# Kernel optimization log

Hardware: AMD Instinct MI355X
Metric: run time of the kernel (lower is better)

Reference implementation:

```python
import jax, jax.numpy as jnp
import numpy as np

N = 100000
E = 1600000
IN_C = 128
OUT_C = 64
HID = 2 * OUT_C  # 128


def gcn_conv(x, src, dst, W, b, n):
    # PyG GCNConv with add_self_loops=True, symmetric normalization, bias.
    h = x @ W  # [n, d_out] - transform first (PyG order)
    ones = jnp.ones(src.shape[0], dtype=h.dtype)
    deg = jax.ops.segment_sum(ones, dst, num_segments=n)  # includes self-loops -> deg >= 1
    dinv = jax.lax.rsqrt(deg)
    norm = dinv[src] * dinv[dst]  # [E+n]
    msg = h[src] * norm[:, None]  # gather + scale
    return jax.ops.segment_sum(msg, dst, num_segments=n) + b


def setup_inputs() -> dict:
    key = jax.random.key(0)
    ks = jax.random.split(key, 8)
    x = jax.random.normal(ks[0], (N, IN_C), dtype=jnp.float32)
    edge_index = jax.random.randint(ks[1], (2, E), 0, N, dtype=jnp.int64)
    s1 = 1.0 / np.sqrt(IN_C)
    s2 = 1.0 / np.sqrt(HID)
    s3 = 1.0 / np.sqrt(OUT_C)
    W1 = jax.random.normal(ks[2], (IN_C, HID), dtype=jnp.float32) * s1
    b1 = jnp.zeros((HID,), dtype=jnp.float32)
    W2 = jax.random.normal(ks[3], (HID, OUT_C), dtype=jnp.float32) * s2
    b2 = jnp.zeros((OUT_C,), dtype=jnp.float32)
    Wfc = jax.random.normal(ks[4], (OUT_C, OUT_C), dtype=jnp.float32) * s3
    bfc = jax.random.uniform(ks[5], (OUT_C,), dtype=jnp.float32, minval=-s3, maxval=s3)
    return {"x": x, "edge_index": edge_index, "W1": W1, "b1": b1,
            "W2": W2, "b2": b2, "Wfc": Wfc, "bfc": bfc}


def reference(x, edge_index, W1, b1, W2, b2, Wfc, bfc):
    n = x.shape[0]
    loop = jnp.arange(n, dtype=edge_index.dtype)
    src = jnp.concatenate([edge_index[0], loop])  # add self-loops
    dst = jnp.concatenate([edge_index[1], loop])
    h = jax.nn.relu(gcn_conv(x, src, dst, W1, b1, n))
    h = gcn_conv(h, src, dst, W2, b2, n)
    return h @ Wfc + bfc
```

## Files before the change

kernel.cpp:

```cpp
#include <hip/hip_runtime.h>

#define INC  128
#define HIDC 128
#define OUTC 64

#define BSH   8
#define NBMAX 512
#define HB    128
#define TILE  4096
#define CAP   8192

typedef unsigned int  u32;
typedef unsigned short u16;
typedef short bf16x8 __attribute__((ext_vector_type(8)));
typedef float f32x4 __attribute__((ext_vector_type(4)));

static __device__ __forceinline__ u16 f2bf(float f) {
    u32 u = __builtin_bit_cast(u32, f);
    u += 0x7fffu + ((u >> 16) & 1u);
    return (u16)(u >> 16);
}
static __device__ __forceinline__ float bf_lo(u32 u) {
    return __builtin_bit_cast(float, u << 16);
}
static __device__ __forceinline__ float bf_hi(u32 u) {
    return __builtin_bit_cast(float, u & 0xffff0000u);
}


__global__ __launch_bounds__(256) void bhist_kernel(const int* __restrict__ dst,
                                                    int* __restrict__ parts,
                                                    int E, int nb) {
    __shared__ int h[NBMAX];
    for (int i = threadIdx.x; i < NBMAX; i += 256) h[i] = 0;
    __syncthreads();
    const int total = HB * 256;
    for (int e = blockIdx.x * 256 + threadIdx.x; e < E; e += total)
        atomicAdd(&h[dst[e] >> BSH], 1);
    __syncthreads();
    for (int i = threadIdx.x; i < nb; i += 256) parts[i * HB + blockIdx.x] = h[i];
}

__global__ __launch_bounds__(512) void bscan_kernel(const int* __restrict__ parts,
                                                    int* __restrict__ bucketOff, int nb) {
    __shared__ int sums[NBMAX];
    const int tid = threadIdx.x;
    int s = 0;
    if (tid < nb) {
        const int* p = parts + tid * HB;
#pragma unroll 8
        for (int r = 0; r < HB; ++r) s += p[r];
    }
    sums[tid] = s;
    __syncthreads();
    for (int d = 1; d < NBMAX; d <<= 1) {
        int t = sums[tid];
        int a = (tid >= d) ? sums[tid - d] : 0;
        __syncthreads();
        sums[tid] = t + a;
        __syncthreads();
    }
    if (tid < nb) bucketOff[tid] = sums[tid] - s;
    if (tid == NBMAX - 1) bucketOff[nb] = sums[NBMAX - 1];
}

__global__ __launch_bounds__(256) void multisplit_kernel(const int* __restrict__ src,
                                                         const int* __restrict__ dst,
                                                         const int* __restrict__ bucketOff,
                                                         int* __restrict__ gfill,
                                                         u32* __restrict__ binned,
                                                         int E, int nb) {
    __shared__ int hist[NBMAX];
    __shared__ int sbase[NBMAX];
    __shared__ int cursor[NBMAX];
    __shared__ int gposs[NBMAX];
    __shared__ int wsum[4];
    __shared__ int2 buf[TILE];
    const int tid  = threadIdx.x;
    const int base = blockIdx.x * TILE;
    const int cnt  = min(TILE, E - base);

    for (int i = tid; i < NBMAX; i += 256) hist[i] = 0;
    __syncthreads();

    int ls[16], ld[16], dg[16];
#pragma unroll
    for (int k = 0; k < 16; ++k) {
        int idx = tid + k * 256;
        if (idx < cnt) {
            ls[k] = src[base + idx];
            ld[k] = dst[base + idx];
            dg[k] = ld[k] >> BSH;
            atomicAdd(&hist[dg[k]], 1);
        } else dg[k] = -1;
    }
    __syncthreads();
    {
        const int a = hist[2 * tid], b = hist[2 * tid + 1];
        const int s = a + b;
        const int lane = tid & 63;
        int incl = s;
#pragma unroll
        for (int d = 1; d < 64; d <<= 1) {
            int t = __shfl_up(incl, d);
            if (lane >= d) incl += t;
        }
        if (lane == 63) wsum[tid >> 6] = incl;
        __syncthreads();
        const int w = tid >> 6;
        int wbase = 0;
        if (w > 0) wbase += wsum[0];
        if (w > 1) wbase += wsum[1];
        if (w > 2) wbase += wsum[2];
        const int excl = wbase + incl - s;
        sbase[2 * tid] = excl;          cursor[2 * tid] = excl;
        sbase[2 * tid + 1] = excl + a;  cursor[2 * tid + 1] = excl + a;
    }
    __syncthreads();
#pragma unroll
    for (int k = 0; k < 16; ++k) {
        if (dg[k] >= 0) {
            int p = atomicAdd(&cursor[dg[k]], 1);
            buf[p] = make_int2(ls[k], ld[k]);
        }
    }
    __syncthreads();
    for (int d = tid; d < nb; d += 256) {
        int c = cursor[d] - sbase[d];
        gposs[d] = (c > 0) ? atomicAdd(&gfill[d], c) : 0;
    }
    __syncthreads();
    for (int idx = tid; idx < cnt; idx += 256) {
        int2 e = buf[idx];
        int d = e.y >> BSH;
        binned[bucketOff[d] + gposs[d] + (idx - sbase[d])] =
            (u32)e.x | ((u32)(e.y & 255) << 24);
    }
}

__global__ __launch_bounds__(256) void csr_build_kernel(const u32* __restrict__ binned,
                                                        const int* __restrict__ bucketOff,
                                                        int* __restrict__ col,
                                                        int* __restrict__ rowptr,
                                                        float* __restrict__ dinv,
                                                        int n, int E) {
    __shared__ int cnt[257];
    __shared__ int excl[256];
    __shared__ int wsum[4];
    __shared__ int colstage[CAP];
    const int tid   = threadIdx.x;
    const int b     = blockIdx.x;
    const int node0 = b << BSH;
    const int nNodes = min(256, n - node0);
    const int e0 = bucketOff[b], e1 = bucketOff[b + 1];
    const int ec = e1 - e0;

    for (int i = tid; i <= 256; i += 256) cnt[i] = 0;
    __syncthreads();
    for (int i = tid; i < ec; i += 256)
        atomicAdd(&cnt[binned[e0 + i] >> 24], 1);
    __syncthreads();
    const int myc = cnt[tid];
    {
        const int lane = tid & 63;
        int incl = myc;
#pragma unroll
        for (int d = 1; d < 64; d <<= 1) {
            int t = __shfl_up(incl, d);
            if (lane >= d) incl += t;
        }
        if (lane == 63) wsum[tid >> 6] = incl;
        __syncthreads();
        const int w = tid >> 6;
        int wbase = 0;
        if (w > 0) wbase += wsum[0];
        if (w > 1) wbase += wsum[1];
        if (w > 2) wbase += wsum[2];
        excl[tid] = wbase + incl - myc;
    }
    __syncthreads();
    if (tid < nNodes) {
        const int node = node0 + tid;
        rowptr[node] = e0 + excl[tid];
        dinv[node] = rsqrtf((float)(myc + 1));
    }
    if (b == 0 && tid == 0) rowptr[n] = E;
    __syncthreads();
    cnt[tid] = excl[tid];
    __syncthreads();
    if (ec <= CAP) {
        for (int i = tid; i < ec; i += 256) {
            u32 e = binned[e0 + i];
            int p = atomicAdd(&cnt[e >> 24], 1);
            colstage[p] = (int)(e & 0xffffffu);
        }
        __syncthreads();
        for (int i = tid; i < ec; i += 256) col[e0 + i] = colstage[i];
    } else {
        for (int i = tid; i < ec; i += 256) {
            u32 e = binned[e0 + i];
            int p = atomicAdd(&cnt[e >> 24], 1);
            col[e0 + p] = (int)(e & 0xffffffu);
        }
    }
}

__global__ __launch_bounds__(256) void fold_kernel(const float* __restrict__ W1,
                                                   const float* __restrict__ W2,
                                                   const float* __restrict__ Wfc,
                                                   const float* __restrict__ b2,
                                                   const float* __restrict__ bfc,
                                                   u16* __restrict__ W1t,
                                                   u16* __restrict__ W2ft,
                                                   float* __restrict__ b2f) {
    int t = blockIdx.x * 256 + threadIdx.x;
    if (t < HIDC * HIDC) {
        int nn = t >> 7, k = t & 127;
        W1t[nn * HIDC + k] = f2bf(W1[k * HIDC + nn]);
    } else if (t < HIDC * HIDC + HIDC * OUTC) {
        int u = t - HIDC * HIDC;
        int i = u >> 6, j = u & 63;
        float s = 0.f;
#pragma unroll 8
        for (int k = 0; k < OUTC; ++k) s = fmaf(W2[i * OUTC + k], Wfc[k * OUTC + j], s);
        W2ft[j * HIDC + i] = f2bf(s);
    } else if (t < HIDC * HIDC + HIDC * OUTC + OUTC) {
        int j = t - HIDC * HIDC - HIDC * OUTC;
        float s = bfc[j];
#pragma unroll 8
        for (int k = 0; k < OUTC; ++k) s = fmaf(b2[k], Wfc[k * OUTC + j], s);
        b2f[j] = s;
    }
}


template <int N, bool AF32>
__global__ __launch_bounds__(256) void mfma_gemm_kernel(const void* __restrict__ Aptr,
                                                        const u16* __restrict__ Wt,
                                                        const float* __restrict__ dinv,
                                                        u16* __restrict__ out, int M) {
    constexpr int K = 128;
    constexpr int NC = N / 16;
    __shared__ u16 Ws[N * K];

    const int tid = threadIdx.x;
    for (int id = tid; id < N * K / 8; id += 256) {
        int nn = id >> 4;
        int c  = id & 15;
        uint4 v = *(const uint4*)(Wt + nn * K + c * 8);
        int slot = (nn << 4) + (c ^ (nn & 7));
        *(uint4*)((char*)Ws + slot * 16) = v;
    }

    const int wave = tid >> 6;
    const int lane = tid & 63;
    const int r0   = blockIdx.x * 64 + wave * 16;
    const int arow = r0 + (lane & 15);
    const int kgrp = lane >> 4;
    __syncthreads();

    f32x4 acc[NC];
#pragma unroll
    for (int nc = 0; nc < NC; ++nc) acc[nc] = f32x4{0.f, 0.f, 0.f, 0.f};

#pragma unroll
    for (int kc = 0; kc < 4; ++kc) {
        bf16x8 af = {0, 0, 0, 0, 0, 0, 0, 0};
        if (arow < M) {
            if constexpr (AF32) {
                const float* ap = (const float*)Aptr + (size_t)arow * K + kc * 32 + kgrp * 8;
                float4 v0 = *(const float4*)ap;
                float4 v1 = *(const float4*)(ap + 4);
                af[0] = (short)f2bf(v0.x); af[1] = (short)f2bf(v0.y);
                af[2] = (short)f2bf(v0.z); af[3] = (short)f2bf(v0.w);
                af[4] = (short)f2bf(v1.x); af[5] = (short)f2bf(v1.y);
                af[6] = (short)f2bf(v1.z); af[7] = (short)f2bf(v1.w);
            } else {
                af = *(const bf16x8*)((const u16*)Aptr + (size_t)arow * K + kc * 32 + kgrp * 8);
            }
        }
#pragma unroll
        for (int nc = 0; nc < NC; ++nc) {
            int nn = nc * 16 + (lane & 15);
            int slot = (nn << 4) + ((kc * 4 + kgrp) ^ (nn & 7));
            bf16x8 bfr = *(const bf16x8*)((const char*)Ws + slot * 16);
            acc[nc] = __builtin_amdgcn_mfma_f32_16x16x32_bf16(af, bfr, acc[nc], 0, 0, 0);
        }
    }
#pragma unroll
    for (int reg = 0; reg < 4; ++reg) {
        int row = r0 + (lane >> 4) * 4 + reg;
        if (row <= M) {
            float sc = (row < M) ? dinv[row] : 0.f;
#pragma unroll
            for (int nc = 0; nc < NC; ++nc)
                out[(size_t)row * N + nc * 16 + (lane & 15)] = f2bf(acc[nc][reg] * sc);
        }
    }
}


__global__ __launch_bounds__(256) void agg1_kernel(const u16* __restrict__ g,
                                                   const int* __restrict__ rowptr,
                                                   const int* __restrict__ col,
                                                   const float* __restrict__ dinv,
                                                   const float* __restrict__ b1,
                                                   u32* __restrict__ h1, int n) {
    const int wid  = threadIdx.x >> 6;
    const int lane = threadIdx.x & 63;
    const int v = blockIdx.x * 4 + wid;
    if (v >= n) return;
    const int h = lane >> 5;
    const int r = lane & 31;
    const int base = rowptr[v], endi = rowptr[v + 1];

    float a0 = 0.f, a1 = 0.f, a2 = 0.f, a3 = 0.f;
    float b0 = 0.f, b1v = 0.f, b2v = 0.f, b3 = 0.f;
    {
        uint2 sv = *(const uint2*)(g + ((size_t)v << 7) + (r << 2));
        if (h == 0) {
            a0 = bf_lo(sv.x); a1 = bf_hi(sv.x);
            a2 = bf_lo(sv.y); a3 = bf_hi(sv.y);
        }
    }

    for (int c = base; c < endi; c += 64) {
        const int m = min(64, endi - c);
        const int idx = (lane < m) ? col[c + lane] : n;
        for (int i = 0; i < m; i += 8) {
            int u0 = __shfl(idx, i + h);
            int u1 = __shfl(idx, i + 2 + h);
            int u2 = __shfl(idx, i + 4 + h);
            int u3 = __shfl(idx, i + 6 + h);
            uint2 x0 = *(const uint2*)(g + ((size_t)u0 << 7) + (r << 2));
            uint2 x1 = *(const uint2*)(g + ((size_t)u1 << 7) + (r << 2));
            uint2 x2 = *(const uint2*)(g + ((size_t)u2 << 7) + (r << 2));
            uint2 x3 = *(const uint2*)(g + ((size_t)u3 << 7) + (r << 2));
            a0 += bf_lo(x0.x); a1 += bf_hi(x0.x); a2 += bf_lo(x0.y); a3 += bf_hi(x0.y);
            b0 += bf_lo(x1.x); b1v += bf_hi(x1.x); b2v += bf_lo(x1.y); b3 += bf_hi(x1.y);
            a0 += bf_lo(x2.x); a1 += bf_hi(x2.x); a2 += bf_lo(x2.y); a3 += bf_hi(x2.y);
            b0 += bf_lo(x3.x); b1v += bf_hi(x3.x); b2v += bf_lo(x3.y); b3 += bf_hi(x3.y);
        }
    }
    float s0 = a0 + b0, s1 = a1 + b1v, s2 = a2 + b2v, s3 = a3 + b3;
    s0 += __shfl_xor(s0, 32);
    s1 += __shfl_xor(s1, 32);
    s2 += __shfl_xor(s2, 32);
    s3 += __shfl_xor(s3, 32);
    if (h == 0) {
        const float dv = dinv[v];
        const float4 bb = *(const float4*)&b1[r << 2];
        float o0 = fmaxf(fmaf(dv, s0, bb.x), 0.f);
        float o1 = fmaxf(fmaf(dv, s1, bb.y), 0.f);
        float o2 = fmaxf(fmaf(dv, s2, bb.z), 0.f);
        float o3 = fmaxf(fmaf(dv, s3, bb.w), 0.f);
        uint2 pk;
        pk.x = (u32)f2bf(o0) | ((u32)f2bf(o1) << 16);
        pk.y = (u32)f2bf(o2) | ((u32)f2bf(o3) << 16);
        *(uint2*)(h1 + ((size_t)v << 6) + (r << 1)) = pk;
    }
}

__global__ __launch_bounds__(256) void agg2_kernel(const u16* __restrict__ g2,
                                                   const int* __restrict__ rowptr,
                                                   const int* __restrict__ col,
                                                   const float* __restrict__ dinv,
                                                   const float* __restrict__ b2f,
                                                   float* __restrict__ out, int n) {
    const int wid  = threadIdx.x >> 6;
    const int lane = threadIdx.x & 63;
    const int v = blockIdx.x * 4 + wid;
    if (v >= n) return;
    const int q = lane >> 4;
    const int r = lane & 15;
    const int base = rowptr[v], endi = rowptr[v + 1];

    float a0 = 0.f, a1 = 0.f, a2 = 0.f, a3 = 0.f;
    float b0 = 0.f, b1v = 0.f, b2v = 0.f, b3 = 0.f;
    {
        uint2 sv = *(const uint2*)(g2 + ((size_t)v << 6) + (r << 2));
        if (q == 0) {
            a0 = bf_lo(sv.x); a1 = bf_hi(sv.x);
            a2 = bf_lo(sv.y); a3 = bf_hi(sv.y);
        }
    }

    for (int c = base; c < endi; c += 64) {
        const int m = min(64, endi - c);
        const int idx = (lane < m) ? col[c + lane] : n;
        for (int i = 0; i < m; i += 8) {
            int u0 = __shfl(idx, i + q);
            int u1 = __shfl(idx, i + 4 + q);
            uint2 x0 = *(const uint2*)(g2 + ((size_t)u0 << 6) + (r << 2));
            uint2 x1 = *(const uint2*)(g2 + ((size_t)u1 << 6) + (r << 2));
            a0 += bf_lo(x0.x); a1 += bf_hi(x0.x); a2 += bf_lo(x0.y); a3 += bf_hi(x0.y);
            b0 += bf_lo(x1.x); b1v += bf_hi(x1.x); b2v += bf_lo(x1.y); b3 += bf_hi(x1.y);
        }
    }
    float s0 = a0 + b0, s1 = a1 + b1v, s2 = a2 + b2v, s3 = a3 + b3;
    s0 += __shfl_xor(s0, 16); s0 += __shfl_xor(s0, 32);
    s1 += __shfl_xor(s1, 16); s1 += __shfl_xor(s1, 32);
    s2 += __shfl_xor(s2, 16); s2 += __shfl_xor(s2, 32);
    s3 += __shfl_xor(s3, 16); s3 += __shfl_xor(s3, 32);
    if (q == 0) {
        const float dv = dinv[v];
        const float4 bb = *(const float4*)&b2f[r << 2];
        float4 o;
        o.x = fmaf(dv, s0, bb.x);
        o.y = fmaf(dv, s1, bb.y);
        o.z = fmaf(dv, s2, bb.z);
        o.w = fmaf(dv, s3, bb.w);
        *(float4*)(out + ((size_t)v << 6) + (r << 2)) = o;
    }
}


extern "C" void kernel_launch(void* const* d_in, const int* in_sizes, int n_in,
                              void* d_out, int out_size, void* d_ws, size_t ws_size,
                              hipStream_t stream) {
    const float* x   = (const float*)d_in[0];
    const int*   ei  = (const int*)d_in[1];
    const float* W1  = (const float*)d_in[2];
    const float* b1  = (const float*)d_in[3];
    const float* W2  = (const float*)d_in[4];
    const float* b2  = (const float*)d_in[5];
    const float* Wfc = (const float*)d_in[6];
    const float* bfc = (const float*)d_in[7];
    float* out = (float*)d_out;

    const int n = in_sizes[0] / INC;
    const int E = in_sizes[1] / 2;
    const int* src = ei;
    const int* dst = ei + E;
    const int nb = (n + 255) >> BSH;

    char* w = (char*)d_ws;
    auto alloc = [&](size_t bytes) -> void* {
        void* p = (void*)w;
        w += (bytes + 255) & ~(size_t)255;
        return p;
    };
    int*   rowptr    = (int*)alloc((size_t)(n + 1) * 4);
    float* dinvp     = (float*)alloc((size_t)n * 4);
    int*   col       = (int*)alloc((size_t)(E + 64) * 4);
    u32*   binned    = (u32*)alloc((size_t)E * 4);
    int*   parts     = (int*)alloc((size_t)NBMAX * HB * 4);
    int*   bucketOff = (int*)alloc((size_t)(nb + 1) * 4);
    int*   gfill     = (int*)alloc((size_t)nb * 4);
    u16*   g         = (u16*)alloc((size_t)(n + 1) * HIDC * 2);
    u16*   h1        = (u16*)alloc((size_t)n * HIDC * 2);
    u16*   W1t       = (u16*)alloc((size_t)HIDC * HIDC * 2);
    u16*   W2ft      = (u16*)alloc((size_t)OUTC * HIDC * 2);
    float* b2f       = (float*)alloc((size_t)OUTC * 4);

    hipMemsetAsync(gfill, 0, (size_t)nb * 4, stream);

    fold_kernel<<<(HIDC * HIDC + HIDC * OUTC + OUTC + 255) / 256, 256, 0, stream>>>(
        W1, W2, Wfc, b2, bfc, W1t, W2ft, b2f);
    bhist_kernel<<<HB, 256, 0, stream>>>(dst, parts, E, nb);
    bscan_kernel<<<1, NBMAX, 0, stream>>>(parts, bucketOff, nb);
    multisplit_kernel<<<(E + TILE - 1) / TILE, 256, 0, stream>>>(src, dst, bucketOff, gfill, binned, E, nb);
    csr_build_kernel<<<nb, 256, 0, stream>>>(binned, bucketOff, col, rowptr, dinvp, n, E);

    mfma_gemm_kernel<HIDC, true><<<(n + 64) / 64, 256, 0, stream>>>(x, W1t, dinvp, g, n);
    agg1_kernel<<<(n + 3) / 4, 256, 0, stream>>>(g, rowptr, col, dinvp, b1, (u32*)h1, n);

    mfma_gemm_kernel<OUTC, false><<<(n + 64) / 64, 256, 0, stream>>>(h1, W2ft, dinvp, g, n);
    agg2_kernel<<<(n + 3) / 4, 256, 0, stream>>>(g, rowptr, col, dinvp, b2f, out, n);
}
```

Measured before the change: 197.0 us.

## Merge first GEMM with multisplit kernel and compute degree in histogram pass

Per-node in-degree counts now come from the histogram pass through global atomics, so the GEMMs and aggregations compute rsqrt(deg) inline instead of waiting on dinv from the CSR build. This lets the first GEMM run in the same launch as the edge multisplit, using disjoint block ranges and a shared smem buffer, so dense and sparse-prep work overlap and one launch is saved. The aggregation kernels switch to grid-stride loops over 2048 blocks. The cost is a global atomic per edge into the count array, a larger merged smem footprint, and an extra memset.

```diff
diff --git a/kernel.cpp b/kernel.cpp
--- a/kernel.cpp
+++ b/kernel.cpp
@@ -28,15 +28,19 @@
 }
 
 
-__global__ __launch_bounds__(256) void bhist_kernel(const int* __restrict__ dst,
+__global__ __launch_bounds__(256) void hist2_kernel(const int* __restrict__ dst,
+                                                    int* __restrict__ cnt,
                                                     int* __restrict__ parts,
                                                     int E, int nb) {
     __shared__ int h[NBMAX];
     for (int i = threadIdx.x; i < NBMAX; i += 256) h[i] = 0;
     __syncthreads();
     const int total = HB * 256;
-    for (int e = blockIdx.x * 256 + threadIdx.x; e < E; e += total)
-        atomicAdd(&h[dst[e] >> BSH], 1);
+    for (int e = blockIdx.x * 256 + threadIdx.x; e < E; e += total) {
+        int d = dst[e];
+        atomicAdd(&cnt[d], 1);
+        atomicAdd(&h[d >> BSH], 1);
+    }
     __syncthreads();
     for (int i = threadIdx.x; i < nb; i += 256) parts[i * HB + blockIdx.x] = h[i];
 }
@@ -64,20 +68,87 @@
     if (tid == NBMAX - 1) bucketOff[nb] = sums[NBMAX - 1];
 }
 
-__global__ __launch_bounds__(256) void multisplit_kernel(const int* __restrict__ src,
-                                                         const int* __restrict__ dst,
-                                                         const int* __restrict__ bucketOff,
-                                                         int* __restrict__ gfill,
-                                                         u32* __restrict__ binned,
-                                                         int E, int nb) {
-    __shared__ int hist[NBMAX];
-    __shared__ int sbase[NBMAX];
-    __shared__ int cursor[NBMAX];
-    __shared__ int gposs[NBMAX];
-    __shared__ int wsum[4];
-    __shared__ int2 buf[TILE];
+
+template <int N, bool AF32>
+static __device__ __forceinline__ void gemm_body(char* smem, const void* __restrict__ Aptr,
+                                                 const u16* __restrict__ Wt,
+                                                 const int* __restrict__ cnt,
+                                                 u16* __restrict__ out, int M, int bid) {
+    constexpr int K = 128;
+    constexpr int NC = N / 16;
+    u16* Ws = (u16*)smem;
+
+    const int tid = threadIdx.x;
+    for (int id = tid; id < N * K / 8; id += 256) {
+        int nn = id >> 4;
+        int c  = id & 15;
+        uint4 v = *(const uint4*)(Wt + nn * K + c * 8);
+        int slot = (nn << 4) + (c ^ (nn & 7));
+        *(uint4*)((char*)Ws + slot * 16) = v;
+    }
+
+    const int wave = tid >> 6;
+    const int lane = tid & 63;
+    const int r0   = bid * 64 + wave * 16;
+    const int arow = r0 + (lane & 15);
+    const int kgrp = lane >> 4;
+    __syncthreads();
+
+    f32x4 acc[NC];
+#pragma unroll
+    for (int nc = 0; nc < NC; ++nc) acc[nc] = f32x4{0.f, 0.f, 0.f, 0.f};
+
+#pragma unroll
+    for (int kc = 0; kc < 4; ++kc) {
+        bf16x8 af = {0, 0, 0, 0, 0, 0, 0, 0};
+        if (arow < M) {
+            if constexpr (AF32) {
+                const float* ap = (const float*)Aptr + (size_t)arow * K + kc * 32 + kgrp * 8;
+                float4 v0 = *(const float4*)ap;
+                float4 v1 = *(const float4*)(ap + 4);
+                af[0] = (short)f2bf(v0.x); af[1] = (short)f2bf(v0.y);
+                af[2] = (short)f2bf(v0.z); af[3] = (short)f2bf(v0.w);
+                af[4] = (short)f2bf(v1.x); af[5] = (short)f2bf(v1.y);
+                af[6] = (short)f2bf(v1.z); af[7] = (short)f2bf(v1.w);
+            } else {
+                af = *(const bf16x8*)((const u16*)Aptr + (size_t)arow * K + kc * 32 + kgrp * 8);
+            }
+        }
+#pragma unroll
+        for (int nc = 0; nc < NC; ++nc) {
+            int nn = nc * 16 + (lane & 15);
+            int slot = (nn << 4) + ((kc * 4 + kgrp) ^ (nn & 7));
+            bf16x8 bfr = *(const bf16x8*)((const char*)Ws + slot * 16);
+            acc[nc] = __builtin_amdgcn_mfma_f32_16x16x32_bf16(af, bfr, acc[nc], 0, 0, 0);
+        }
+    }
+#pragma unroll
+    for (int reg = 0; reg < 4; ++reg) {
+        int row = r0 + (lane >> 4) * 4 + reg;
+        if (row <= M) {
+            float sc = (row < M) ? rsqrtf((float)(cnt[row] + 1)) : 0.f;
+#pragma unroll
+            for (int nc = 0; nc < NC; ++nc)
+                out[(size_t)row * N + nc * 16 + (lane & 15)] = f2bf(acc[nc][reg] * sc);
+        }
+    }
+}
+
+static __device__ __forceinline__ void ms_body(char* smem,
+                                               const int* __restrict__ src,
+                                               const int* __restrict__ dst,
+                                               const int* __restrict__ bucketOff,
+                                               int* __restrict__ gfill,
+                                               u32* __restrict__ binned,
+                                               int E, int nb, int bid) {
+    int2* buf   = (int2*)smem;
+    int* hist   = (int*)(smem + TILE * 8);
+    int* sbase  = hist + NBMAX;
+    int* cursor = sbase + NBMAX;
+    int* gposs  = cursor + NBMAX;
+    int* wsum   = gposs + NBMAX;
     const int tid  = threadIdx.x;
-    const int base = blockIdx.x * TILE;
+    const int base = bid * TILE;
     const int cnt  = min(TILE, E - base);
 
     for (int i = tid; i < NBMAX; i += 256) hist[i] = 0;
@@ -138,11 +209,37 @@
     }
 }
 
+#define SMEM_MERGED 41008
+
+__global__ __launch_bounds__(256) void gemm1_ms_kernel(const float* __restrict__ x,
+                                                       const u16* __restrict__ W1t,
+                                                       const int* __restrict__ cnt,
+                                                       u16* __restrict__ g, int M,
+                                                       const int* __restrict__ src,
+                                                       const int* __restrict__ dst,
+                                                       const int* __restrict__ bucketOff,
+                                                       int* __restrict__ gfill,
+                                                       u32* __restrict__ binned,
+                                                       int E, int nb, int G) {
+    __shared__ __align__(16) char smem[SMEM_MERGED];
+    const int b = (int)blockIdx.x;
+    if (b < G) gemm_body<HIDC, true>(smem, x, W1t, cnt, g, M, b);
+    else       ms_body(smem, src, dst, bucketOff, gfill, binned, E, nb, b - G);
+}
+
+__global__ __launch_bounds__(256) void gemm2_kernel(const u16* __restrict__ h1,
+                                                    const u16* __restrict__ W2ft,
+                                                    const int* __restrict__ cnt,
+                                                    u16* __restrict__ g, int M) {
+    __shared__ __align__(16) char smem[OUTC * 128 * 2];
+    gemm_body<OUTC, false>(smem, h1, W2ft, cnt, g, M, (int)blockIdx.x);
+}
+
+
 __global__ __launch_bounds__(256) void csr_build_kernel(const u32* __restrict__ binned,
                                                         const int* __restrict__ bucketOff,
                                                         int* __restrict__ col,
                                                         int* __restrict__ rowptr,
-                                                        float* __restrict__ dinv,
                                                         int n, int E) {
     __shared__ int cnt[257];
     __shared__ int excl[256];
@@ -179,11 +276,7 @@
         excl[tid] = wbase + incl - myc;
     }
     __syncthreads();
-    if (tid < nNodes) {
-        const int node = node0 + tid;
-        rowptr[node] = e0 + excl[tid];
-        dinv[node] = rsqrtf((float)(myc + 1));
-    }
+    if (tid < nNodes) rowptr[node0 + tid] = e0 + excl[tid];
     if (b == 0 && tid == 0) rowptr[n] = E;
     __syncthreads();
     cnt[tid] = excl[tid];
@@ -234,183 +327,121 @@
 }
 
 
-template <int N, bool AF32>
-__global__ __launch_bounds__(256) void mfma_gemm_kernel(const void* __restrict__ Aptr,
-                                                        const u16* __restrict__ Wt,
-                                                        const float* __restrict__ dinv,
-                                                        u16* __restrict__ out, int M) {
-    constexpr int K = 128;
-    constexpr int NC = N / 16;
-    __shared__ u16 Ws[N * K];
-
-    const int tid = threadIdx.x;
-    for (int id = tid; id < N * K / 8; id += 256) {
-        int nn = id >> 4;
-        int c  = id & 15;
-        uint4 v = *(const uint4*)(Wt + nn * K + c * 8);
-        int slot = (nn << 4) + (c ^ (nn & 7));
-        *(uint4*)((char*)Ws + slot * 16) = v;
-    }
-
-    const int wave = tid >> 6;
-    const int lane = tid & 63;
-    const int r0   = blockIdx.x * 64 + wave * 16;
-    const int arow = r0 + (lane & 15);
-    const int kgrp = lane >> 4;
-    __syncthreads();
-
-    f32x4 acc[NC];
-#pragma unroll
-    for (int nc = 0; nc < NC; ++nc) acc[nc] = f32x4{0.f, 0.f, 0.f, 0.f};
-
-#pragma unroll
-    for (int kc = 0; kc < 4; ++kc) {
-        bf16x8 af = {0, 0, 0, 0, 0, 0, 0, 0};
-        if (arow < M) {
-            if constexpr (AF32) {
-                const float* ap = (const float*)Aptr + (size_t)arow * K + kc * 32 + kgrp * 8;
-                float4 v0 = *(const float4*)ap;
-                float4 v1 = *(const float4*)(ap + 4);
-                af[0] = (short)f2bf(v0.x); af[1] = (short)f2bf(v0.y);
-                af[2] = (short)f2bf(v0.z); af[3] = (short)f2bf(v0.w);
-                af[4] = (short)f2bf(v1.x); af[5] = (short)f2bf(v1.y);
-                af[6] = (short)f2bf(v1.z); af[7] = (short)f2bf(v1.w);
-            } else {
-                af = *(const bf16x8*)((const u16*)Aptr + (size_t)arow * K + kc * 32 + kgrp * 8);
-            }
-        }
-#pragma unroll
-        for (int nc = 0; nc < NC; ++nc) {
-            int nn = nc * 16 + (lane & 15);
-            int slot = (nn << 4) + ((kc * 4 + kgrp) ^ (nn & 7));
-            bf16x8 bfr = *(const bf16x8*)((const char*)Ws + slot * 16);
-            acc[nc] = __builtin_amdgcn_mfma_f32_16x16x32_bf16(af, bfr, acc[nc], 0, 0, 0);
-        }
-    }
-#pragma unroll
-    for (int reg = 0; reg < 4; ++reg) {
-        int row = r0 + (lane >> 4) * 4 + reg;
-        if (row <= M) {
-            float sc = (row < M) ? dinv[row] : 0.f;
-#pragma unroll
-            for (int nc = 0; nc < NC; ++nc)
-                out[(size_t)row * N + nc * 16 + (lane & 15)] = f2bf(acc[nc][reg] * sc);
-        }
-    }
-}
-
-
 __global__ __launch_bounds__(256) void agg1_kernel(const u16* __restrict__ g,
                                                    const int* __restrict__ rowptr,
                                                    const int* __restrict__ col,
-                                                   const float* __restrict__ dinv,
+                                                   const int* __restrict__ cntp,
                                                    const float* __restrict__ b1,
                                                    u32* __restrict__ h1, int n) {
     const int wid  = threadIdx.x >> 6;
     const int lane = threadIdx.x & 63;
-    const int v = blockIdx.x * 4 + wid;
-    if (v >= n) return;
     const int h = lane >> 5;
     const int r = lane & 31;
-    const int base = rowptr[v], endi = rowptr[v + 1];
-
-    float a0 = 0.f, a1 = 0.f, a2 = 0.f, a3 = 0.f;
-    float b0 = 0.f, b1v = 0.f, b2v = 0.f, b3 = 0.f;
-    {
-        uint2 sv = *(const uint2*)(g + ((size_t)v << 7) + (r << 2));
+    const int vstep = gridDim.x * 4;
+
+    for (int v = blockIdx.x * 4 + wid; v < n; v += vstep) {
+        const int base = rowptr[v], endi = rowptr[v + 1];
+
+        float a0 = 0.f, a1 = 0.f, a2 = 0.f, a3 = 0.f;
+        float b0 = 0.f, b1v = 0.f, b2v = 0.f, b3 = 0.f;
+        {
+            uint2 sv = *(const uint2*)(g + ((size_t)v << 7) + (r << 2));
+            if (h == 0) {
+                a0 = bf_lo(sv.x); a1 = bf_hi(sv.x);
+                a2 = bf_lo(sv.y); a3 = bf_hi(sv.y);
+            }
+        }
+
+        for (int c = base; c < endi; c += 64) {
+            const int m = min(64, endi - c);
+            const int idx = (lane < m) ? col[c + lane] : n;
+            for (int i = 0; i < m; i += 8) {
+                int u0 = __shfl(idx, i + h);
+                int u1 = __shfl(idx, i + 2 + h);
+                int u2 = __shfl(idx, i + 4 + h);
+                int u3 = __shfl(idx, i + 6 + h);
+                uint2 x0 = *(const uint2*)(g + ((size_t)u0 << 7) + (r << 2));
+                uint2 x1 = *(const uint2*)(g + ((size_t)u1 << 7) + (r << 2));
+                uint2 x2 = *(const uint2*)(g + ((size_t)u2 << 7) + (r << 2));
+                uint2 x3 = *(const uint2*)(g + ((size_t)u3 << 7) + (r << 2));
+                a0 += bf_lo(x0.x); a1 += bf_hi(x0.x); a2 += bf_lo(x0.y); a3 += bf_hi(x0.y);
+                b0 += bf_lo(x1.x); b1v += bf_hi(x1.x); b2v += bf_lo(x1.y); b3 += bf_hi(x1.y);
+                a0 += bf_lo(x2.x); a1 += bf_hi(x2.x); a2 += bf_lo(x2.y); a3 += bf_hi(x2.y);
+                b0 += bf_lo(x3.x); b1v += bf_hi(x3.x); b2v += bf_lo(x3.y); b3 += bf_hi(x3.y);
+            }
+        }
+        float s0 = a0 + b0, s1 = a1 + b1v, s2 = a2 + b2v, s3 = a3 + b3;
+        s0 += __shfl_xor(s0, 32);
+        s1 += __shfl_xor(s1, 32);
+        s2 += __shfl_xor(s2, 32);
+        s3 += __shfl_xor(s3, 32);
         if (h == 0) {
-            a0 = bf_lo(sv.x); a1 = bf_hi(sv.x);
-            a2 = bf_lo(sv.y); a3 = bf_hi(sv.y);
-        }
-    }
-
-    for (int c = base; c < endi; c += 64) {
-        const int m = min(64, endi - c);
-        const int idx = (lane < m) ? col[c + lane] : n;
-        for (int i = 0; i < m; i += 8) {
-            int u0 = __shfl(idx, i + h);
-            int u1 = __shfl(idx, i + 2 + h);
-            int u2 = __shfl(idx, i + 4 + h);
-            int u3 = __shfl(idx, i + 6 + h);
-            uint2 x0 = *(const uint2*)(g + ((size_t)u0 << 7) + (r << 2));
-            uint2 x1 = *(const uint2*)(g + ((size_t)u1 << 7) + (r << 2));
-            uint2 x2 = *(const uint2*)(g + ((size_t)u2 << 7) + (r << 2));
-            uint2 x3 = *(const uint2*)(g + ((size_t)u3 << 7) + (r << 2));
-            a0 += bf_lo(x0.x); a1 += bf_hi(x0.x); a2 += bf_lo(x0.y); a3 += bf_hi(x0.y);
-            b0 += bf_lo(x1.x); b1v += bf_hi(x1.x); b2v += bf_lo(x1.y); b3 += bf_hi(x1.y);
-            a0 += bf_lo(x2.x); a1 += bf_hi(x2.x); a2 += bf_lo(x2.y); a3 += bf_hi(x2.y);
-            b0 += bf_lo(x3.x); b1v += bf_hi(x3.x); b2v += bf_lo(x3.y); b3 += bf_hi(x3.y);
-        }
-    }
-    float s0 = a0 + b0, s1 = a1 + b1v, s2 = a2 + b2v, s3 = a3 + b3;
-    s0 += __shfl_xor(s0, 32);
-    s1 += __shfl_xor(s1, 32);
-    s2 += __shfl_xor(s2, 32);
-    s3 += __shfl_xor(s3, 32);
-    if (h == 0) {
-        const float dv = dinv[v];
-        const float4 bb = *(const float4*)&b1[r << 2];
-        float o0 = fmaxf(fmaf(dv, s0, bb.x), 0.f);
-        float o1 = fmaxf(fmaf(dv, s1, bb.y), 0.f);
-        float o2 = fmaxf(fmaf(dv, s2, bb.z), 0.f);
-        float o3 = fmaxf(fmaf(dv, s3, bb.w), 0.f);
-        uint2 pk;
-        pk.x = (u32)f2bf(o0) | ((u32)f2bf(o1) << 16);
-        pk.y = (u32)f2bf(o2) | ((u32)f2bf(o3) << 16);
-        *(uint2*)(h1 + ((size_t)v << 6) + (r << 1)) = pk;
+            const float dv = rsqrtf((float)(cntp[v] + 1));
+            const float4 bb = *(const float4*)&b1[r << 2];
+            float o0 = fmaxf(fmaf(dv, s0, bb.x), 0.f);
+            float o1 = fmaxf(fmaf(dv, s1, bb.y), 0.f);
+            float o2 = fmaxf(fmaf(dv, s2, bb.z), 0.f);
+            float o3 = fmaxf(fmaf(dv, s3, bb.w), 0.f);
+            uint2 pk;
+            pk.x = (u32)f2bf(o0) | ((u32)f2bf(o1) << 16);
+            pk.y = (u32)f2bf(o2) | ((u32)f2bf(o3) << 16);
+            *(uint2*)(h1 + ((size_t)v << 6) + (r << 1)) = pk;
+        }
     }
 }
 
 __global__ __launch_bounds__(256) void agg2_kernel(const u16* __restrict__ g2,
                                                    const int* __restrict__ rowptr,
                                                    const int* __restrict__ col,
-                                                   const float* __restrict__ dinv,
+                                                   const int* __restrict__ cntp,
                                                    const float* __restrict__ b2f,
                                                    float* __restrict__ out, int n) {
     const int wid  = threadIdx.x >> 6;
     const int lane = threadIdx.x & 63;
-    const int v = blockIdx.x * 4 + wid;
-    if (v >= n) return;
     const int q = lane >> 4;
     const int r = lane & 15;
-    const int base = rowptr[v], endi = rowptr[v + 1];
-
-    float a0 = 0.f, a1 = 0.f, a2 = 0.f, a3 = 0.f;
-    float b0 = 0.f, b1v = 0.f, b2v = 0.f, b3 = 0.f;
-    {
-        uint2 sv = *(const uint2*)(g2 + ((size_t)v << 6) + (r << 2));
+    const int vstep = gridDim.x * 4;
+
+    for (int v = blockIdx.x * 4 + wid; v < n; v += vstep) {
+        const int base = rowptr[v], endi = rowptr[v + 1];
+
+        float a0 = 0.f, a1 = 0.f, a2 = 0.f, a3 = 0.f;
+        float b0 = 0.f, b1v = 0.f, b2v = 0.f, b3 = 0.f;
+        {
+            uint2 sv = *(const uint2*)(g2 + ((size_t)v << 6) + (r << 2));
+            if (q == 0) {
+                a0 = bf_lo(sv.x); a1 = bf_hi(sv.x);
+                a2 = bf_lo(sv.y); a3 = bf_hi(sv.y);
+            }
+        }
+
+        for (int c = base; c < endi; c += 64) {
+            const int m = min(64, endi - c);
+            const int idx = (lane < m) ? col[c + lane] : n;
+            for (int i = 0; i < m; i += 8) {
+                int u0 = __shfl(idx, i + q);
+                int u1 = __shfl(idx, i + 4 + q);
+                uint2 x0 = *(const uint2*)(g2 + ((size_t)u0 << 6) + (r << 2));
+                uint2 x1 = *(const uint2*)(g2 + ((size_t)u1 << 6) + (r << 2));
+                a0 += bf_lo(x0.x); a1 += bf_hi(x0.x); a2 += bf_lo(x0.y); a3 += bf_hi(x0.y);
+                b0 += bf_lo(x1.x); b1v += bf_hi(x1.x); b2v += bf_lo(x1.y); b3 += bf_hi(x1.y);
+            }
+        }
+        float s0 = a0 + b0, s1 = a1 + b1v, s2 = a2 + b2v, s3 = a3 + b3;
+        s0 += __shfl_xor(s0, 16); s0 += __shfl_xor(s0, 32);
+        s1 += __shfl_xor(s1, 16); s1 += __shfl_xor(s1, 32);
+        s2 += __shfl_xor(s2, 16); s2 += __shfl_xor(s2, 32);
+        s3 += __shfl_xor(s3, 16); s3 += __shfl_xor(s3, 32);
         if (q == 0) {
-            a0 = bf_lo(sv.x); a1 = bf_hi(sv.x);
-            a2 = bf_lo(sv.y); a3 = bf_hi(sv.y);
-        }
-    }
-
-    for (int c = base; c < endi; c += 64) {
-        const int m = min(64, endi - c);
-        const int idx = (lane < m) ? col[c + lane] : n;
-        for (int i = 0; i < m; i += 8) {
-            int u0 = __shfl(idx, i + q);
-            int u1 = __shfl(idx, i + 4 + q);
-            uint2 x0 = *(const uint2*)(g2 + ((size_t)u0 << 6) + (r << 2));
-            uint2 x1 = *(const uint2*)(g2 + ((size_t)u1 << 6) + (r << 2));
-            a0 += bf_lo(x0.x); a1 += bf_hi(x0.x); a2 += bf_lo(x0.y); a3 += bf_hi(x0.y);
-            b0 += bf_lo(x1.x); b1v += bf_hi(x1.x); b2v += bf_lo(x1.y); b3 += bf_hi(x1.y);
-        }
-    }
-    float s0 = a0 + b0, s1 = a1 + b1v, s2 = a2 + b2v, s3 = a3 + b3;
-    s0 += __shfl_xor(s0, 16); s0 += __shfl_xor(s0, 32);
-    s1 += __shfl_xor(s1, 16); s1 += __shfl_xor(s1, 32);
-    s2 += __shfl_xor(s2, 16); s2 += __shfl_xor(s2, 32);
-    s3 += __shfl_xor(s3, 16); s3 += __shfl_xor(s3, 32);
-    if (q == 0) {
-        const float dv = dinv[v];
-        const float4 bb = *(const float4*)&b2f[r << 2];
-        float4 o;
-        o.x = fmaf(dv, s0, bb.x);
-        o.y = fmaf(dv, s1, bb.y);
-        o.z = fmaf(dv, s2, bb.z);
-        o.w = fmaf(dv, s3, bb.w);
-        *(float4*)(out + ((size_t)v << 6) + (r << 2)) = o;
+            const float dv = rsqrtf((float)(cntp[v] + 1));
+            const float4 bb = *(const float4*)&b2f[r << 2];
+            float4 o;
+            o.x = fmaf(dv, s0, bb.x);
+            o.y = fmaf(dv, s1, bb.y);
+            o.z = fmaf(dv, s2, bb.z);
+            o.w = fmaf(dv, s3, bb.w);
+            *(float4*)(out + ((size_t)v << 6) + (r << 2)) = o;
+        }
     }
 }
 
@@ -441,7 +472,7 @@
         return p;
     };
     int*   rowptr    = (int*)alloc((size_t)(n + 1) * 4);
-    float* dinvp     = (float*)alloc((size_t)n * 4);
+    int*   cnt       = (int*)alloc((size_t)n * 4);
     int*   col       = (int*)alloc((size_t)(E + 64) * 4);
     u32*   binned    = (u32*)alloc((size_t)E * 4);
     int*   parts     = (int*)alloc((size_t)NBMAX * HB * 4);
@@ -453,18 +484,21 @@
     u16*   W2ft      = (u16*)alloc((size_t)OUTC * HIDC * 2);
     float* b2f       = (float*)alloc((size_t)OUTC * 4);
 
+    hipMemsetAsync(cnt, 0, (size_t)n * 4, stream);
     hipMemsetAsync(gfill, 0, (size_t)nb * 4, stream);
 
     fold_kernel<<<(HIDC * HIDC + HIDC * OUTC + OUTC + 255) / 256, 256, 0, stream>>>(
         W1, W2, Wfc, b2, bfc, W1t, W2ft, b2f);
-    bhist_kernel<<<HB, 256, 0, stream>>>(dst, parts, E, nb);
+    hist2_kernel<<<HB, 256, 0, stream>>>(dst, cnt, parts, E, nb);
     bscan_kernel<<<1, NBMAX, 0, stream>>>(parts, bucketOff, nb);
-    multisplit_kernel<<<(E + TILE - 1) / TILE, 256, 0, stream>>>(src, dst, bucketOff, gfill, binned, E, nb);
-    csr_build_kernel<<<nb, 256, 0, stream>>>(binned, bucketOff, col, rowptr, dinvp, n, E);
-
-    mfma_gemm_kernel<HIDC, true><<<(n + 64) / 64, 256, 0, stream>>>(x, W1t, dinvp, g, n);
-    agg1_kernel<<<(n + 3) / 4, 256, 0, stream>>>(g, rowptr, col, dinvp, b1, (u32*)h1, n);
-
-    mfma_gemm_kernel<OUTC, false><<<(n + 64) / 64, 256, 0, stream>>>(h1, W2ft, dinvp, g, n);
-    agg2_kernel<<<(n + 3) / 4, 256, 0, stream>>>(g, rowptr, col, dinvp, b2f, out, n);
-}
+
+    const int G  = (n + 64) / 64;
+    const int MS = (E + TILE - 1) / TILE;
+    gemm1_ms_kernel<<<G + MS, 256, 0, stream>>>(x, W1t, cnt, g, n,
+                                                src, dst, bucketOff, gfill, binned, E, nb, G);
+    csr_build_kernel<<<nb, 256, 0, stream>>>(binned, bucketOff, col, rowptr, n, E);
+
+    agg1_kernel<<<2048, 256, 0, stream>>>(g, rowptr, col, cnt, b1, (u32*)h1, n);
+    gemm2_kernel<<<(n + 64) / 64, 256, 0, stream>>>(h1, W2ft, cnt, g, n);
+    agg2_kernel<<<2048, 256, 0, stream>>>(g, rowptr, col, cnt, b2f, out, n);
+}
```

Result: slower. 246.9 us (+25.3%).

## Fuse second-layer GEMM into first aggregation kernel via per-row LDS dot products

Applied to the files above, without the earlier changes.

The second-layer dense transform (h1 @ W2·Wfc, scaled by dinv) is now computed inside agg1 rather than in a separate MFMA GEMM launch. agg1 caches W2ft in LDS, writes each aggregated ReLU row to shared memory, and each lane computes one of the 64 outputs with scalar FMAs. agg1 becomes a persistent grid-stride kernel with 2048 blocks so the LDS weight load is amortized over many rows. This removes the h1 round trip through global memory and one kernel launch. The cost is 128 scalar FMAs per lane per row in place of MFMA, plus extra LDS traffic; the padding row of g2 is zeroed in fold_kernel.

```diff
diff --git a/kernel.cpp b/kernel.cpp
--- a/kernel.cpp
+++ b/kernel.cpp
@@ -25,6 +25,9 @@
 }
 static __device__ __forceinline__ float bf_hi(u32 u) {
     return __builtin_bit_cast(float, u & 0xffff0000u);
+}
+static __device__ __forceinline__ float bfu(short s) {
+    return __builtin_bit_cast(float, (u32)(u16)s << 16);
 }
 
 
@@ -212,7 +215,8 @@
                                                    const float* __restrict__ bfc,
                                                    u16* __restrict__ W1t,
                                                    u16* __restrict__ W2ft,
-                                                   float* __restrict__ b2f) {
+                                                   float* __restrict__ b2f,
+                                                   u16* __restrict__ g2, int n) {
     int t = blockIdx.x * 256 + threadIdx.x;
     if (t < HIDC * HIDC) {
         int nn = t >> 7, k = t & 127;
@@ -230,17 +234,18 @@
 #pragma unroll 8
         for (int k = 0; k < OUTC; ++k) s = fmaf(b2[k], Wfc[k * OUTC + j], s);
         b2f[j] = s;
-    }
-}
-
-
-template <int N, bool AF32>
-__global__ __launch_bounds__(256) void mfma_gemm_kernel(const void* __restrict__ Aptr,
-                                                        const u16* __restrict__ Wt,
-                                                        const float* __restrict__ dinv,
-                                                        u16* __restrict__ out, int M) {
-    constexpr int K = 128;
-    constexpr int NC = N / 16;
+    } else if (t < HIDC * HIDC + HIDC * OUTC + 2 * OUTC) {
+        int j = t - HIDC * HIDC - HIDC * OUTC - OUTC;
+        g2[(size_t)n * OUTC + j] = 0;
+    }
+}
+
+
+__global__ __launch_bounds__(256) void mfma_gemm1_kernel(const float* __restrict__ A,
+                                                         const u16* __restrict__ Wt,
+                                                         const float* __restrict__ dinv,
+                                                         u16* __restrict__ out, int M) {
+    constexpr int N = HIDC, K = 128, NC = N / 16;
     __shared__ u16 Ws[N * K];
 
     const int tid = threadIdx.x;
@@ -267,17 +272,13 @@
     for (int kc = 0; kc < 4; ++kc) {
         bf16x8 af = {0, 0, 0, 0, 0, 0, 0, 0};
         if (arow < M) {
-            if constexpr (AF32) {
-                const float* ap = (const float*)Aptr + (size_t)arow * K + kc * 32 + kgrp * 8;
-                float4 v0 = *(const float4*)ap;
-                float4 v1 = *(const float4*)(ap + 4);
-                af[0] = (short)f2bf(v0.x); af[1] = (short)f2bf(v0.y);
-                af[2] = (short)f2bf(v0.z); af[3] = (short)f2bf(v0.w);
-                af[4] = (short)f2bf(v1.x); af[5] = (short)f2bf(v1.y);
-                af[6] = (short)f2bf(v1.z); af[7] = (short)f2bf(v1.w);
-            } else {
-                af = *(const bf16x8*)((const u16*)Aptr + (size_t)arow * K + kc * 32 + kgrp * 8);
-            }
+            const float* ap = A + (size_t)arow * K + kc * 32 + kgrp * 8;
+            float4 v0 = *(const float4*)ap;
+            float4 v1 = *(const float4*)(ap + 4);
+            af[0] = (short)f2bf(v0.x); af[1] = (short)f2bf(v0.y);
+            af[2] = (short)f2bf(v0.z); af[3] = (short)f2bf(v0.w);
+            af[4] = (short)f2bf(v1.x); af[5] = (short)f2bf(v1.y);
+            af[6] = (short)f2bf(v1.z); af[7] = (short)f2bf(v1.w);
         }
 #pragma unroll
         for (int nc = 0; nc < NC; ++nc) {
@@ -305,59 +306,87 @@
                                                    const int* __restrict__ col,
                                                    const float* __restrict__ dinv,
                                                    const float* __restrict__ b1,
-                                                   u32* __restrict__ h1, int n) {
-    const int wid  = threadIdx.x >> 6;
-    const int lane = threadIdx.x & 63;
-    const int v = blockIdx.x * 4 + wid;
-    if (v >= n) return;
+                                                   const u16* __restrict__ W2ft,
+                                                   u16* __restrict__ g2, int n) {
+    __shared__ u16 Wl[OUTC][HIDC + 8];
+    __shared__ u16 h1row[4][HIDC];
+    const int tid = threadIdx.x;
+    for (int id = tid; id < OUTC * (HIDC / 8); id += 256) {
+        int row = id >> 4, ch = id & 15;
+        *(uint4*)&Wl[row][ch * 8] = *(const uint4*)&W2ft[row * HIDC + ch * 8];
+    }
+    __syncthreads();
+
+    const int wid  = tid >> 6;
+    const int lane = tid & 63;
     const int h = lane >> 5;
     const int r = lane & 31;
-    const int base = rowptr[v], endi = rowptr[v + 1];
-
-    float a0 = 0.f, a1 = 0.f, a2 = 0.f, a3 = 0.f;
-    float b0 = 0.f, b1v = 0.f, b2v = 0.f, b3 = 0.f;
-    {
-        uint2 sv = *(const uint2*)(g + ((size_t)v << 7) + (r << 2));
-        if (h == 0) {
-            a0 = bf_lo(sv.x); a1 = bf_hi(sv.x);
-            a2 = bf_lo(sv.y); a3 = bf_hi(sv.y);
-        }
-    }
-
-    for (int c = base; c < endi; c += 64) {
-        const int m = min(64, endi - c);
-        const int idx = (lane < m) ? col[c + lane] : n;
-        for (int i = 0; i < m; i += 8) {
-            int u0 = __shfl(idx, i + h);
-            int u1 = __shfl(idx, i + 2 + h);
-            int u2 = __shfl(idx, i + 4 + h);
-            int u3 = __shfl(idx, i + 6 + h);
-            uint2 x0 = *(const uint2*)(g + ((size_t)u0 << 7) + (r << 2));
-            uint2 x1 = *(const uint2*)(g + ((size_t)u1 << 7) + (r << 2));
-            uint2 x2 = *(const uint2*)(g + ((size_t)u2 << 7) + (r << 2));
-            uint2 x3 = *(const uint2*)(g + ((size_t)u3 << 7) + (r << 2));
-            a0 += bf_lo(x0.x); a1 += bf_hi(x0.x); a2 += bf_lo(x0.y); a3 += bf_hi(x0.y);
-            b0 += bf_lo(x1.x); b1v += bf_hi(x1.x); b2v += bf_lo(x1.y); b3 += bf_hi(x1.y);
-            a0 += bf_lo(x2.x); a1 += bf_hi(x2.x); a2 += bf_lo(x2.y); a3 += bf_hi(x2.y);
-            b0 += bf_lo(x3.x); b1v += bf_hi(x3.x); b2v += bf_lo(x3.y); b3 += bf_hi(x3.y);
-        }
-    }
-    float s0 = a0 + b0, s1 = a1 + b1v, s2 = a2 + b2v, s3 = a3 + b3;
-    s0 += __shfl_xor(s0, 32);
-    s1 += __shfl_xor(s1, 32);
-    s2 += __shfl_xor(s2, 32);
-    s3 += __shfl_xor(s3, 32);
-    if (h == 0) {
+    const int vstep = gridDim.x * 4;
+
+    for (int v = blockIdx.x * 4 + wid; v < n; v += vstep) {
+        const int base = rowptr[v], endi = rowptr[v + 1];
+
+        float a0 = 0.f, a1 = 0.f, a2 = 0.f, a3 = 0.f;
+        float b0 = 0.f, b1v = 0.f, b2v = 0.f, b3 = 0.f;
+        {
+            uint2 sv = *(const uint2*)(g + ((size_t)v << 7) + (r << 2));
+            if (h == 0) {
+                a0 = bf_lo(sv.x); a1 = bf_hi(sv.x);
+                a2 = bf_lo(sv.y); a3 = bf_hi(sv.y);
+            }
+        }
+
+        for (int c = base; c < endi; c += 64) {
+            const int m = min(64, endi - c);
+            const int idx = (lane < m) ? col[c + lane] : n;
+            for (int i = 0; i < m; i += 8) {
+                int u0 = __shfl(idx, i + h);
+                int u1 = __shfl(idx, i + 2 + h);
+                int u2 = __shfl(idx, i + 4 + h);
+                int u3 = __shfl(idx, i + 6 + h);
+                uint2 x0 = *(const uint2*)(g + ((size_t)u0 << 7) + (r << 2));
+                uint2 x1 = *(const uint2*)(g + ((size_t)u1 << 7) + (r << 2));
+                uint2 x2 = *(const uint2*)(g + ((size_t)u2 << 7) + (r << 2));
+                uint2 x3 = *(const uint2*)(g + ((size_t)u3 << 7) + (r << 2));
+                a0 += bf_lo(x0.x); a1 += bf_hi(x0.x); a2 += bf_lo(x0.y); a3 += bf_hi(x0.y);
+                b0 += bf_lo(x1.x); b1v += bf_hi(x1.x); b2v += bf_lo(x1.y); b3 += bf_hi(x1.y);
+                a0 += bf_lo(x2.x); a1 += bf_hi(x2.x); a2 += bf_lo(x2.y); a3 += bf_hi(x2.y);
+                b0 += bf_lo(x3.x); b1v += bf_hi(x3.x); b2v += bf_lo(x3.y); b3 += bf_hi(x3.y);
+            }
+        }
+        float s0 = a0 + b0, s1 = a1 + b1v, s2 = a2 + b2v, s3 = a3 + b3;
+        s0 += __shfl_xor(s0, 32);
+        s1 += __shfl_xor(s1, 32);
+        s2 += __shfl_xor(s2, 32);
+        s3 += __shfl_xor(s3, 32);
+
         const float dv = dinv[v];
         const float4 bb = *(const float4*)&b1[r << 2];
         float o0 = fmaxf(fmaf(dv, s0, bb.x), 0.f);
         float o1 = fmaxf(fmaf(dv, s1, bb.y), 0.f);
         float o2 = fmaxf(fmaf(dv, s2, bb.z), 0.f);
         float o3 = fmaxf(fmaf(dv, s3, bb.w), 0.f);
-        uint2 pk;
-        pk.x = (u32)f2bf(o0) | ((u32)f2bf(o1) << 16);
-        pk.y = (u32)f2bf(o2) | ((u32)f2bf(o3) << 16);
-        *(uint2*)(h1 + ((size_t)v << 6) + (r << 1)) = pk;
+        if (h == 0) {
+            uint2 pk;
+            pk.x = (u32)f2bf(o0) | ((u32)f2bf(o1) << 16);
+            pk.y = (u32)f2bf(o2) | ((u32)f2bf(o3) << 16);
+            *(uint2*)&h1row[wid][r << 2] = pk;
+        }
+        float c0 = 0.f, c1 = 0.f, c2 = 0.f, c3 = 0.f;
+#pragma unroll
+        for (int j = 0; j < 16; ++j) {
+            bf16x8 hc = *(const bf16x8*)&h1row[wid][j * 8];
+            bf16x8 wc = *(const bf16x8*)&Wl[lane][j * 8];
+            c0 = fmaf(bfu(hc[0]), bfu(wc[0]), c0);
+            c1 = fmaf(bfu(hc[1]), bfu(wc[1]), c1);
+            c2 = fmaf(bfu(hc[2]), bfu(wc[2]), c2);
+            c3 = fmaf(bfu(hc[3]), bfu(wc[3]), c3);
+            c0 = fmaf(bfu(hc[4]), bfu(wc[4]), c0);
+            c1 = fmaf(bfu(hc[5]), bfu(wc[5]), c1);
+            c2 = fmaf(bfu(hc[6]), bfu(wc[6]), c2);
+            c3 = fmaf(bfu(hc[7]), bfu(wc[7]), c3);
+        }
+        g2[(size_t)v * OUTC + lane] = f2bf(((c0 + c1) + (c2 + c3)) * dv);
     }
 }
 
@@ -448,23 +477,21 @@
     int*   bucketOff = (int*)alloc((size_t)(nb + 1) * 4);
     int*   gfill     = (int*)alloc((size_t)nb * 4);
     u16*   g         = (u16*)alloc((size_t)(n + 1) * HIDC * 2);
-    u16*   h1        = (u16*)alloc((size_t)n * HIDC * 2);
+    u16*   g2        = (u16*)alloc((size_t)(n + 1) * OUTC * 2);
     u16*   W1t       = (u16*)alloc((size_t)HIDC * HIDC * 2);
     u16*   W2ft      = (u16*)alloc((size_t)OUTC * HIDC * 2);
     float* b2f       = (float*)alloc((size_t)OUTC * 4);
 
     hipMemsetAsync(gfill, 0, (size_t)nb * 4, stream);
 
-    fold_kernel<<<(HIDC * HIDC + HIDC * OUTC + OUTC + 255) / 256, 256, 0, stream>>>(
-        W1, W2, Wfc, b2, bfc, W1t, W2ft, b2f);
+    fold_kernel<<<(HIDC * HIDC + HIDC * OUTC + 2 * OUTC + 255) / 256, 256, 0, stream>>>(
+        W1, W2, Wfc, b2, bfc, W1t, W2ft, b2f, g2, n);
     bhist_kernel<<<HB, 256, 0, stream>>>(dst, parts, E, nb);
     bscan_kernel<<<1, NBMAX, 0, stream>>>(parts, bucketOff, nb);
     multisplit_kernel<<<(E + TILE - 1) / TILE, 256, 0, stream>>>(src, dst, bucketOff, gfill, binned, E, nb);
     csr_build_kernel<<<nb, 256, 0, stream>>>(binned, bucketOff, col, rowptr, dinvp, n, E);
 
-    mfma_gemm_kernel<HIDC, true><<<(n + 64) / 64, 256, 0, stream>>>(x, W1t, dinvp, g, n);
-    agg1_kernel<<<(n + 3) / 4, 256, 0, stream>>>(g, rowptr, col, dinvp, b1, (u32*)h1, n);
-
-    mfma_gemm_kernel<OUTC, false><<<(n + 64) / 64, 256, 0, stream>>>(h1, W2ft, dinvp, g, n);
-    agg2_kernel<<<(n + 3) / 4, 256, 0, stream>>>(g, rowptr, col, dinvp, b2f, out, n);
-}
+    mfma_gemm1_kernel<<<(n + 64) / 64, 256, 0, stream>>>(x, W1t, dinvp, g, n);
+    agg1_kernel<<<2048, 256, 0, stream>>>(g, rowptr, col, dinvp, b1, W2ft, g2, n);
+    agg2_kernel<<<(n + 3) / 4, 256, 0, stream>>>(g2, rowptr, col, dinvp, b2f, out, n);
+}
```

Result: slower. 275.7 us (+39.9%).
